# Kernel optimization log

Measured on AMD Instinct MI355X. Metric: run time of the kernel, lower is better.

## Reference

```python
import jax, jax.numpy as jnp
import numpy as np
from jax import lax

N, C_IN, C_OUT, T, V = 16, 256, 256, 300, 25
K = 3            # s_kernel_size
TK = 9           # t_kernel_size
BN_EPS = 1e-5


def setup_inputs() -> dict:
    key = jax.random.key(0)
    ks = jax.random.split(key, 12)
    x = jax.random.normal(ks[0], (N, C_IN, T, V), dtype=jnp.float32)
    A = jax.random.uniform(ks[1], (K, V, V), dtype=jnp.float32)
    att_A = jax.random.uniform(ks[2], (N, 1, V, V), dtype=jnp.float32)  # unused by S_GC
    M = jnp.ones((K, V, V), dtype=jnp.float32)
    # 1x1 spatial conv: out = K*C_OUT channels
    conv_w = jax.random.normal(ks[3], (K * C_OUT, C_IN), dtype=jnp.float32) * 0.02
    conv_b = jnp.zeros((K * C_OUT,), dtype=jnp.float32)
    # BN1 (eval mode)
    bn1_gamma = jnp.ones((C_OUT,), dtype=jnp.float32)
    bn1_beta = jnp.zeros((C_OUT,), dtype=jnp.float32)
    bn1_mean = jax.random.normal(ks[4], (C_OUT,), dtype=jnp.float32) * 0.1
    bn1_var = jax.random.uniform(ks[5], (C_OUT,), dtype=jnp.float32) + 0.5
    # temporal conv: kernel (TK, 1), stride 1, pad ((TK-1)//2, 0)
    tconv_w = jax.random.normal(ks[6], (C_OUT, C_OUT, TK, 1), dtype=jnp.float32) * 0.02
    tconv_b = jnp.zeros((C_OUT,), dtype=jnp.float32)
    # BN2 (eval mode)
    bn2_gamma = jnp.ones((C_OUT,), dtype=jnp.float32)
    bn2_beta = jnp.zeros((C_OUT,), dtype=jnp.float32)
    bn2_mean = jax.random.normal(ks[7], (C_OUT,), dtype=jnp.float32) * 0.1
    bn2_var = jax.random.uniform(ks[8], (C_OUT,), dtype=jnp.float32) + 0.5
    return {
        "x": x, "A": A, "att_A": att_A, "M": M,
        "conv_w": conv_w, "conv_b": conv_b,
        "bn1_gamma": bn1_gamma, "bn1_beta": bn1_beta, "bn1_mean": bn1_mean, "bn1_var": bn1_var,
        "tconv_w": tconv_w, "tconv_b": tconv_b,
        "bn2_gamma": bn2_gamma, "bn2_beta": bn2_beta, "bn2_mean": bn2_mean, "bn2_var": bn2_var,
    }


def _bn(x, gamma, beta, mean, var):
    # eval-mode BatchNorm2d over channel dim of NCHW tensor
    scale = gamma / jnp.sqrt(var + BN_EPS)
    return x * scale[None, :, None, None] + (beta - mean * scale)[None, :, None, None]


def reference(x, A, att_A, M, conv_w, conv_b,
              bn1_gamma, bn1_beta, bn1_mean, bn1_var,
              tconv_w, tconv_b,
              bn2_gamma, bn2_beta, bn2_mean, bn2_var):
    # --- S_GC: 1x1 conv -> view (n,K,c,t,v) -> einsum with A*M ---
    y = jnp.einsum('nctv,oc->notv', x, conv_w) + conv_b[None, :, None, None]
    y = y.reshape(N, K, C_OUT, T, V)
    sgc = jnp.einsum('nkctv,kvw->nctw', y, A * M)
    # --- tgc: BN -> ReLU -> temporal conv -> BN -> Dropout(0) -> ReLU ---
    h = jax.nn.relu(_bn(sgc, bn1_gamma, bn1_beta, bn1_mean, bn1_var))
    h = lax.conv_general_dilated(
        h, tconv_w, window_strides=(1, 1),
        padding=(((TK - 1) // 2, (TK - 1) // 2), (0, 0)),
        dimension_numbers=('NCHW', 'OIHW', 'NCHW'))
    h = h + tconv_b[None, :, None, None]
    h = jax.nn.relu(_bn(h, bn2_gamma, bn2_beta, bn2_mean, bn2_var))
    # --- residual: identity (in_channels == out_channels, stride == 1) ---
    return h + x
```

## Files before the change

kernel.cpp:

```cpp
#include <hip/hip_runtime.h>
#include <math.h>

constexpr int TVL = 7500;
constexpr int CIN = 256;
constexpr int CO  = 256;
constexpr int KO  = 768;
constexpr int KK3 = 2304;
#define BNEPS 1e-5f

typedef __attribute__((ext_vector_type(8))) short short8;
typedef __attribute__((ext_vector_type(4))) float f32x4;
typedef unsigned short ushortT;

static __device__ __forceinline__ ushortT f2bf(float v) {
    unsigned x = __float_as_uint(v);
    unsigned r = (x + 0x7fffu + ((x >> 16) & 1u)) >> 16;
    return (ushortT)r;
}
static __device__ __forceinline__ float bf2f(ushortT u) {
    return __uint_as_float((unsigned)u << 16);
}

static __device__ __forceinline__ void gll16(const void* g, void* l) {
    __builtin_amdgcn_global_load_lds(
        (const __attribute__((address_space(1))) void*)g,
        (__attribute__((address_space(3))) void*)l, 16, 0, 0);
}

__global__ void ksplit_w1(const float* __restrict__ w,
                          ushortT* __restrict__ dH, ushortT* __restrict__ dL,
                          ushortT* __restrict__ zb)
{
    if (blockIdx.x == 0 && threadIdx.x < 16) zb[threadIdx.x] = 0;
    int i = blockIdx.x * 256 + threadIdx.x;
    if (i < KO * CIN) {
        float v = w[i];
        ushortT h = f2bf(v);
        dH[i] = h;
        dL[i] = f2bf(v - bf2f(h));
    }
}

__global__ void ksplit_w3(const float* __restrict__ w,
                          ushortT* __restrict__ dH, ushortT* __restrict__ dL)
{
    int i = blockIdx.x * 256 + threadIdx.x;
    if (i < CO * KK3) {
        int o = i / KK3, rem = i - o * KK3;
        int c = rem / 9, dt = rem - c * 9;
        float v = w[i];
        ushortT h = f2bf(v);
        int j = o * KK3 + dt * 256 + c;
        dH[j] = h;
        dL[j] = f2bf(v - bf2f(h));
    }
}

__global__ __launch_bounds__(256) void ktrans_split(
    const float* __restrict__ src, ushortT* __restrict__ dH, ushortT* __restrict__ dL)
{
    __shared__ float tile[32][33];
    const int z = blockIdx.z;
    src += (size_t)z * CO * TVL;
    dH  += (size_t)z * TVL * 256;
    dL  += (size_t)z * TVL * 256;
    const int tx = threadIdx.x & 31, ty = threadIdx.x >> 5;
    const int wBase = blockIdx.x * 32, cBase = blockIdx.y * 32;
    #pragma unroll
    for (int i = 0; i < 4; ++i) {
        int r = ty + i * 8;
        int w = wBase + tx;
        tile[r][tx] = (w < TVL) ? src[(size_t)(cBase + r) * TVL + w] : 0.f;
    }
    __syncthreads();
    #pragma unroll
    for (int i = 0; i < 4; ++i) {
        int wr = ty + i * 8;
        int w = wBase + wr;
        if (w < TVL) {
            float v = tile[tx][wr];
            ushortT hi = f2bf(v);
            ushortT lo = f2bf(v - bf2f(hi));
            dH[(size_t)w * 256 + cBase + tx] = hi;
            dL[(size_t)w * 256 + cBase + tx] = lo;
        }
    }
}

__global__ __launch_bounds__(256) void k1_mfma(
    const ushortT* __restrict__ Wh, const ushortT* __restrict__ Wl,
    const ushortT* __restrict__ Xh, const ushortT* __restrict__ Xl,
    const ushortT* __restrict__ zb,
    const float* __restrict__ bias, float* __restrict__ out1)
{
    __shared__ __align__(16) short Ah[4096], Al[4096], Bh[4096], Bl[4096];
    const int tid = threadIdx.x;
    const int ng = blockIdx.z;
    const int rowBase = blockIdx.y * 128;
    const int colBase = blockIdx.x * 128;
    const ushortT* XhN = Xh + (size_t)ng * TVL * 256;
    const ushortT* XlN = Xl + (size_t)ng * TVL * 256;

    f32x4 acc[4][4];
    #pragma unroll
    for (int a = 0; a < 4; ++a)
        #pragma unroll
        for (int b = 0; b < 4; ++b) acc[a][b] = (f32x4){0.f, 0.f, 0.f, 0.f};

    const int r0 = tid >> 2, s = tid & 3;
    const int wv = tid >> 6, lane = tid & 63;
    const int wy = wv >> 1, wx = wv & 1;
    const int q = lane >> 4, l15 = lane & 15;
    const int qs0 = s ^ ((r0 >> 1) & 3);
    const int qsr = q ^ ((l15 >> 1) & 3);
    const int ldo0 = tid * 16, ldo1 = 4096 + tid * 16;
    const int bcol0 = colBase + r0, bcol1 = colBase + r0 + 64;

    #pragma unroll 1
    for (int kk = 0; kk < CIN; kk += 32) {
        const size_t goA = (size_t)(rowBase + r0) * CIN + kk + qs0 * 8;
        gll16(Wh + goA, (char*)Ah + ldo0);
        gll16(Wl + goA, (char*)Al + ldo0);
        gll16(Wh + goA + (size_t)64 * CIN, (char*)Ah + ldo1);
        gll16(Wl + goA + (size_t)64 * CIN, (char*)Al + ldo1);

        const size_t goB0 = (size_t)bcol0 * 256 + kk + qs0 * 8;
        const size_t goB1 = (size_t)bcol1 * 256 + kk + qs0 * 8;
        gll16(bcol0 < TVL ? (const void*)(XhN + goB0) : (const void*)zb, (char*)Bh + ldo0);
        gll16(bcol0 < TVL ? (const void*)(XlN + goB0) : (const void*)zb, (char*)Bl + ldo0);
        gll16(bcol1 < TVL ? (const void*)(XhN + goB1) : (const void*)zb, (char*)Bh + ldo1);
        gll16(bcol1 < TVL ? (const void*)(XlN + goB1) : (const void*)zb, (char*)Bl + ldo1);
        __syncthreads();

        short8 ah[4], al[4], bh[4], bl[4];
        #pragma unroll
        for (int mi = 0; mi < 4; ++mi) {
            const int off = (wy * 64 + mi * 16 + l15) * 64 + qsr * 16;
            ah[mi] = *(const short8*)((const char*)Ah + off);
            al[mi] = *(const short8*)((const char*)Al + off);
        }
        #pragma unroll
        for (int ni = 0; ni < 4; ++ni) {
            const int off = (wx * 64 + ni * 16 + l15) * 64 + qsr * 16;
            bh[ni] = *(const short8*)((const char*)Bh + off);
            bl[ni] = *(const short8*)((const char*)Bl + off);
        }
        #pragma unroll
        for (int mi = 0; mi < 4; ++mi)
            #pragma unroll
            for (int ni = 0; ni < 4; ++ni) {
                acc[mi][ni] = __builtin_amdgcn_mfma_f32_16x16x32_bf16(ah[mi], bh[ni], acc[mi][ni], 0, 0, 0);
                acc[mi][ni] = __builtin_amdgcn_mfma_f32_16x16x32_bf16(ah[mi], bl[ni], acc[mi][ni], 0, 0, 0);
                acc[mi][ni] = __builtin_amdgcn_mfma_f32_16x16x32_bf16(al[mi], bh[ni], acc[mi][ni], 0, 0, 0);
            }
        __syncthreads();
    }

    float* out1n = out1 + (size_t)ng * KO * TVL;
    #pragma unroll
    for (int mi = 0; mi < 4; ++mi)
        #pragma unroll
        for (int rr = 0; rr < 4; ++rr) {
            const int row = rowBase + wy * 64 + mi * 16 + q * 4 + rr;
            const float bv = bias[row];
            #pragma unroll
            for (int ni = 0; ni < 4; ++ni) {
                const int col = colBase + wx * 64 + ni * 16 + l15;
                if (col < TVL)
                    out1n[(size_t)row * TVL + col] = acc[mi][ni][rr] + bv;
            }
        }
}

__global__ __launch_bounds__(256) void k2_sgc(
    const float* __restrict__ out1, const float* __restrict__ A,
    const float* __restrict__ Mm, const float* __restrict__ g1,
    const float* __restrict__ b1, const float* __restrict__ m1,
    const float* __restrict__ v1, float* __restrict__ h)
{
    __shared__ __align__(16) float AMs[3 * 25 * 28];
    const int tid = threadIdx.x;
    for (int i = tid; i < 1875; i += 256)
        AMs[(i / 25) * 28 + (i % 25)] = A[i] * Mm[i];
    __syncthreads();

    const int r  = blockIdx.x * 256 + tid;
    const int t2 = r % 150;
    const int rc = r / 150;
    const int c  = rc & 255;
    const int ng = rc >> 8;
    const int t  = t2 * 2;

    const float* base = out1 + ((size_t)ng * KO + c) * TVL + t * 25;
    float o0[25], o1[25];
    #pragma unroll
    for (int w = 0; w < 25; ++w) { o0[w] = 0.f; o1[w] = 0.f; }

    for (int k = 0; k < 3; ++k) {
        const float* yp = base + (size_t)k * CO * TVL;
        float y0[25], y1[25];
        #pragma unroll
        for (int v = 0; v < 25; ++v) { y0[v] = yp[v]; y1[v] = yp[25 + v]; }
        const float* amk = &AMs[k * 25 * 28];
        for (int v = 0; v < 25; ++v) {
            const float* am = amk + v * 28;
            const float ya = y0[v], yb = y1[v];
            #pragma unroll
            for (int w = 0; w < 25; ++w) {
                const float a = am[w];
                o0[w] += ya * a;
                o1[w] += yb * a;
            }
        }
    }

    const float sc = g1[c] / sqrtf(v1[c] + BNEPS);
    const float bi = b1[c] - m1[c] * sc;
    float* hp = h + ((size_t)ng * CO + c) * TVL + t * 25;
    #pragma unroll
    for (int w = 0; w < 25; ++w) {
        const float va = o0[w] * sc + bi;
        const float vb = o1[w] * sc + bi;
        hp[w]      = va > 0.f ? va : 0.f;
        hp[25 + w] = vb > 0.f ? vb : 0.f;
    }
}

__global__ __launch_bounds__(256) void k3_mfma(
    const ushortT* __restrict__ Wh, const ushortT* __restrict__ Wl,
    const ushortT* __restrict__ Hh, const ushortT* __restrict__ Hl,
    const ushortT* __restrict__ zb,
    const float* __restrict__ tb, const float* __restrict__ g2,
    const float* __restrict__ b2, const float* __restrict__ m2,
    const float* __restrict__ v2, const float* __restrict__ x,
    float* __restrict__ out, int n0)
{
    __shared__ __align__(16) short Ah[4096], Al[4096], Bh[4096], Bl[4096];
    const int tid = threadIdx.x;
    const int ng = blockIdx.z;
    const int rowBase = blockIdx.y * 128;
    const int colBase = blockIdx.x * 128;
    const ushortT* HhN = Hh + (size_t)ng * TVL * 256;
    const ushortT* HlN = Hl + (size_t)ng * TVL * 256;

    f32x4 acc[4][4];
    #pragma unroll
    for (int a = 0; a < 4; ++a)
        #pragma unroll
        for (int b = 0; b < 4; ++b) acc[a][b] = (f32x4){0.f, 0.f, 0.f, 0.f};

    const int r0 = tid >> 2, s = tid & 3;
    const int wv = tid >> 6, lane = tid & 63;
    const int wy = wv >> 1, wx = wv & 1;
    const int q = lane >> 4, l15 = lane & 15;
    const int qs0 = s ^ ((r0 >> 1) & 3);
    const int qsr = q ^ ((l15 >> 1) & 3);
    const int ldo0 = tid * 16, ldo1 = 4096 + tid * 16;
    const int bcol0 = colBase + r0, bcol1 = colBase + r0 + 64;

    #pragma unroll 1
    for (int kk = 0; kk < KK3; kk += 32) {
        const int dt = kk >> 8;
        const int c0 = kk & 255;
        const int shift = dt * 25 - 100;

        const size_t goA = (size_t)(rowBase + r0) * KK3 + kk + qs0 * 8;
        gll16(Wh + goA, (char*)Ah + ldo0);
        gll16(Wl + goA, (char*)Al + ldo0);
        gll16(Wh + goA + (size_t)64 * KK3, (char*)Ah + ldo1);
        gll16(Wl + goA + (size_t)64 * KK3, (char*)Al + ldo1);

        const int gcol0 = bcol0 + shift, gcol1 = bcol1 + shift;
        const bool ok0 = (bcol0 < TVL) && ((unsigned)gcol0 < (unsigned)TVL);
        const bool ok1 = (bcol1 < TVL) && ((unsigned)gcol1 < (unsigned)TVL);
        const size_t goB0 = (size_t)gcol0 * 256 + c0 + qs0 * 8;
        const size_t goB1 = (size_t)gcol1 * 256 + c0 + qs0 * 8;
        gll16(ok0 ? (const void*)(HhN + goB0) : (const void*)zb, (char*)Bh + ldo0);
        gll16(ok0 ? (const void*)(HlN + goB0) : (const void*)zb, (char*)Bl + ldo0);
        gll16(ok1 ? (const void*)(HhN + goB1) : (const void*)zb, (char*)Bh + ldo1);
        gll16(ok1 ? (const void*)(HlN + goB1) : (const void*)zb, (char*)Bl + ldo1);
        __syncthreads();

        short8 ah[4], al[4], bh[4], bl[4];
        #pragma unroll
        for (int mi = 0; mi < 4; ++mi) {
            const int off = (wy * 64 + mi * 16 + l15) * 64 + qsr * 16;
            ah[mi] = *(const short8*)((const char*)Ah + off);
            al[mi] = *(const short8*)((const char*)Al + off);
        }
        #pragma unroll
        for (int ni = 0; ni < 4; ++ni) {
            const int off = (wx * 64 + ni * 16 + l15) * 64 + qsr * 16;
            bh[ni] = *(const short8*)((const char*)Bh + off);
            bl[ni] = *(const short8*)((const char*)Bl + off);
        }
        #pragma unroll
        for (int mi = 0; mi < 4; ++mi)
            #pragma unroll
            for (int ni = 0; ni < 4; ++ni) {
                acc[mi][ni] = __builtin_amdgcn_mfma_f32_16x16x32_bf16(ah[mi], bh[ni], acc[mi][ni], 0, 0, 0);
                acc[mi][ni] = __builtin_amdgcn_mfma_f32_16x16x32_bf16(ah[mi], bl[ni], acc[mi][ni], 0, 0, 0);
                acc[mi][ni] = __builtin_amdgcn_mfma_f32_16x16x32_bf16(al[mi], bh[ni], acc[mi][ni], 0, 0, 0);
            }
        __syncthreads();
    }

    const float* xn = x   + (size_t)(n0 + ng) * CO * TVL;
    float*       on = out + (size_t)(n0 + ng) * CO * TVL;
    #pragma unroll
    for (int mi = 0; mi < 4; ++mi)
        #pragma unroll
        for (int rr = 0; rr < 4; ++rr) {
            const int row = rowBase + wy * 64 + mi * 16 + q * 4 + rr;
            const float sc = g2[row] / sqrtf(v2[row] + BNEPS);
            const float bb = (tb[row] - m2[row]) * sc + b2[row];
            #pragma unroll
            for (int ni = 0; ni < 4; ++ni) {
                const int col = colBase + wx * 64 + ni * 16 + l15;
                if (col < TVL) {
                    const size_t o = (size_t)row * TVL + col;
                    on[o] = fmaxf(acc[mi][ni][rr] * sc + bb, 0.f) + xn[o];
                }
            }
        }
}

extern "C" void kernel_launch(void* const* d_in, const int* in_sizes, int n_in,
                              void* d_out, int out_size, void* d_ws, size_t ws_size,
                              hipStream_t stream)
{
    const float* x  = (const float*)d_in[0];
    const float* A  = (const float*)d_in[1];
    const float* Mm = (const float*)d_in[3];
    const float* cw = (const float*)d_in[4];
    const float* cb = (const float*)d_in[5];
    const float* g1 = (const float*)d_in[6];
    const float* b1 = (const float*)d_in[7];
    const float* m1 = (const float*)d_in[8];
    const float* v1 = (const float*)d_in[9];
    const float* tw = (const float*)d_in[10];
    const float* tb = (const float*)d_in[11];
    const float* g2 = (const float*)d_in[12];
    const float* b2 = (const float*)d_in[13];
    const float* m2 = (const float*)d_in[14];
    const float* v2 = (const float*)d_in[15];
    float* out = (float*)d_out;

    ushortT* zb  = (ushortT*)d_ws;
    ushortT* W1h = (ushortT*)((char*)d_ws + 256);
    ushortT* W1l = W1h + KO * CIN;
    ushortT* W3h = W1l + KO * CIN;
    ushortT* W3l = W3h + CO * KK3;
    char* dyn = (char*)(W3l + CO * KK3);
    const size_t fixed = (size_t)(dyn - (char*)d_ws);
    const size_t avail = ws_size > fixed ? ws_size - fixed : 0;
    const size_t perN = (size_t)KO * TVL * 4 + (size_t)CO * TVL * 4
                      + 4 * (size_t)TVL * 256 * 2;
    int g = 16;
    while (g > 1 && (size_t)g * perN > avail) g >>= 1;

    float*   out1 = (float*)dyn;
    float*   hbuf = out1 + (size_t)g * KO * TVL;
    ushortT* Hh   = (ushortT*)(hbuf + (size_t)g * CO * TVL);
    ushortT* Hl   = Hh + (size_t)g * TVL * 256;
    ushortT* Xh   = Hl + (size_t)g * TVL * 256;
    ushortT* Xl   = Xh + (size_t)g * TVL * 256;

    hipLaunchKernelGGL(ksplit_w1, dim3((KO * CIN + 255) / 256), dim3(256), 0, stream, cw, W1h, W1l, zb);
    hipLaunchKernelGGL(ksplit_w3, dim3((CO * KK3 + 255) / 256), dim3(256), 0, stream, tw, W3h, W3l);

    for (int n0 = 0; n0 < 16; n0 += g) {
        hipLaunchKernelGGL(ktrans_split, dim3(235, 8, g), dim3(256), 0, stream,
                           x + (size_t)n0 * CIN * TVL, Xh, Xl);
        hipLaunchKernelGGL(k1_mfma, dim3(59, 6, g), dim3(256), 0, stream,
                           W1h, W1l, Xh, Xl, zb, cb, out1);
        hipLaunchKernelGGL(k2_sgc, dim3(g * 150), dim3(256), 0, stream,
                           out1, A, Mm, g1, b1, m1, v1, hbuf);
        hipLaunchKernelGGL(ktrans_split, dim3(235, 8, g), dim3(256), 0, stream,
                           hbuf, Hh, Hl);
        hipLaunchKernelGGL(k3_mfma, dim3(59, 2, g), dim3(256), 0, stream,
                           W3h, W3l, Hh, Hl, zb, tb, g2, b2, m2, v2, x, out, n0);
    }
}
```

Before: 1.318 ms.

## Double-buffer LDS in MFMA GEMMs, remap blocks across XCDs, reuse workspace buffers

Both bf16x3 MFMA GEMM kernels now use double-buffered LDS: the next K-slice is loaded with global_load_lds while the current slice is computed, which hides load latency and needs one fewer barrier per step. Block indices are remapped so consecutive tiles land on the same XCD, which should improve L2 reuse. k2 writes its output in place into out1 and the transposed H reuses the X split buffers, shrinking the per-batch workspace so larger groups fit. The in-place write drops the restrict qualifiers and relies on each thread reading its inputs before writing, and doubling LDS to 64KB per block may lower occupancy.

```diff
diff --git a/kernel.cpp b/kernel.cpp
--- a/kernel.cpp
+++ b/kernel.cpp
@@ -25,6 +25,21 @@
     __builtin_amdgcn_global_load_lds(
         (const __attribute__((address_space(1))) void*)g,
         (__attribute__((address_space(3))) void*)l, 16, 0, 0);
+}
+
+static __device__ __forceinline__ void xcd_remap(int gx, int gy,
+                                                 int& bx, int& by, int& bz)
+{
+    const int gz = gridDim.z;
+    const int total = gx * gy * gz;
+    const int lin = blockIdx.x + gx * (blockIdx.y + gy * blockIdx.z);
+    const int q = total >> 3, r = total & 7;
+    const int xcd = lin & 7, idx = lin >> 3;
+    const int nl = (xcd < r ? xcd * (q + 1) : r * (q + 1) + (xcd - r) * q) + idx;
+    bx = nl % gx;
+    const int rest = nl / gx;
+    by = rest % gy;
+    bz = rest / gy;
 }
 
 __global__ void ksplit_w1(const float* __restrict__ w,
@@ -57,11 +72,12 @@
 }
 
 __global__ __launch_bounds__(256) void ktrans_split(
-    const float* __restrict__ src, ushortT* __restrict__ dH, ushortT* __restrict__ dL)
+    const float* __restrict__ src, size_t zstr,
+    ushortT* __restrict__ dH, ushortT* __restrict__ dL)
 {
     __shared__ float tile[32][33];
     const int z = blockIdx.z;
-    src += (size_t)z * CO * TVL;
+    src += (size_t)z * zstr;
     dH  += (size_t)z * TVL * 256;
     dL  += (size_t)z * TVL * 256;
     const int tx = threadIdx.x & 31, ty = threadIdx.x >> 5;
@@ -93,11 +109,13 @@
     const ushortT* __restrict__ zb,
     const float* __restrict__ bias, float* __restrict__ out1)
 {
-    __shared__ __align__(16) short Ah[4096], Al[4096], Bh[4096], Bl[4096];
+    __shared__ __align__(16) short Ah[2][4096], Al[2][4096], Bh[2][4096], Bl[2][4096];
     const int tid = threadIdx.x;
-    const int ng = blockIdx.z;
-    const int rowBase = blockIdx.y * 128;
-    const int colBase = blockIdx.x * 128;
+    int bx, by, bz;
+    xcd_remap(gridDim.x, gridDim.y, bx, by, bz);
+    const int ng = bz;
+    const int rowBase = by * 128;
+    const int colBase = bx * 128;
     const ushortT* XhN = Xh + (size_t)ng * TVL * 256;
     const ushortT* XlN = Xl + (size_t)ng * TVL * 256;
 
@@ -116,34 +134,46 @@
     const int ldo0 = tid * 16, ldo1 = 4096 + tid * 16;
     const int bcol0 = colBase + r0, bcol1 = colBase + r0 + 64;
 
+    auto stage = [&](int kk, int p) {
+        short* ahp = Ah[p]; short* alp = Al[p];
+        short* bhp = Bh[p]; short* blp = Bl[p];
+        const size_t goA = (size_t)(rowBase + r0) * CIN + kk + qs0 * 8;
+        gll16(Wh + goA, (char*)ahp + ldo0);
+        gll16(Wl + goA, (char*)alp + ldo0);
+        gll16(Wh + goA + (size_t)64 * CIN, (char*)ahp + ldo1);
+        gll16(Wl + goA + (size_t)64 * CIN, (char*)alp + ldo1);
+        const size_t goB0 = (size_t)bcol0 * 256 + kk + qs0 * 8;
+        const size_t goB1 = (size_t)bcol1 * 256 + kk + qs0 * 8;
+        gll16(bcol0 < TVL ? (const void*)(XhN + goB0) : (const void*)zb, (char*)bhp + ldo0);
+        gll16(bcol0 < TVL ? (const void*)(XlN + goB0) : (const void*)zb, (char*)blp + ldo0);
+        gll16(bcol1 < TVL ? (const void*)(XhN + goB1) : (const void*)zb, (char*)bhp + ldo1);
+        gll16(bcol1 < TVL ? (const void*)(XlN + goB1) : (const void*)zb, (char*)blp + ldo1);
+    };
+
+    stage(0, 0);
+    __syncthreads();
+    int p = 0;
+
     #pragma unroll 1
     for (int kk = 0; kk < CIN; kk += 32) {
-        const size_t goA = (size_t)(rowBase + r0) * CIN + kk + qs0 * 8;
-        gll16(Wh + goA, (char*)Ah + ldo0);
-        gll16(Wl + goA, (char*)Al + ldo0);
-        gll16(Wh + goA + (size_t)64 * CIN, (char*)Ah + ldo1);
-        gll16(Wl + goA + (size_t)64 * CIN, (char*)Al + ldo1);
-
-        const size_t goB0 = (size_t)bcol0 * 256 + kk + qs0 * 8;
-        const size_t goB1 = (size_t)bcol1 * 256 + kk + qs0 * 8;
-        gll16(bcol0 < TVL ? (const void*)(XhN + goB0) : (const void*)zb, (char*)Bh + ldo0);
-        gll16(bcol0 < TVL ? (const void*)(XlN + goB0) : (const void*)zb, (char*)Bl + ldo0);
-        gll16(bcol1 < TVL ? (const void*)(XhN + goB1) : (const void*)zb, (char*)Bh + ldo1);
-        gll16(bcol1 < TVL ? (const void*)(XlN + goB1) : (const void*)zb, (char*)Bl + ldo1);
-        __syncthreads();
-
+        if (kk + 32 < CIN) stage(kk + 32, p ^ 1);
+
+        const char* AhP = (const char*)Ah[p];
+        const char* AlP = (const char*)Al[p];
+        const char* BhP = (const char*)Bh[p];
+        const char* BlP = (const char*)Bl[p];
         short8 ah[4], al[4], bh[4], bl[4];
         #pragma unroll
         for (int mi = 0; mi < 4; ++mi) {
             const int off = (wy * 64 + mi * 16 + l15) * 64 + qsr * 16;
-            ah[mi] = *(const short8*)((const char*)Ah + off);
-            al[mi] = *(const short8*)((const char*)Al + off);
+            ah[mi] = *(const short8*)(AhP + off);
+            al[mi] = *(const short8*)(AlP + off);
         }
         #pragma unroll
         for (int ni = 0; ni < 4; ++ni) {
             const int off = (wx * 64 + ni * 16 + l15) * 64 + qsr * 16;
-            bh[ni] = *(const short8*)((const char*)Bh + off);
-            bl[ni] = *(const short8*)((const char*)Bl + off);
+            bh[ni] = *(const short8*)(BhP + off);
+            bl[ni] = *(const short8*)(BlP + off);
         }
         #pragma unroll
         for (int mi = 0; mi < 4; ++mi)
@@ -154,6 +184,7 @@
                 acc[mi][ni] = __builtin_amdgcn_mfma_f32_16x16x32_bf16(al[mi], bh[ni], acc[mi][ni], 0, 0, 0);
             }
         __syncthreads();
+        p ^= 1;
     }
 
     float* out1n = out1 + (size_t)ng * KO * TVL;
@@ -173,10 +204,10 @@
 }
 
 __global__ __launch_bounds__(256) void k2_sgc(
-    const float* __restrict__ out1, const float* __restrict__ A,
+    const float* out1, const float* __restrict__ A,
     const float* __restrict__ Mm, const float* __restrict__ g1,
     const float* __restrict__ b1, const float* __restrict__ m1,
-    const float* __restrict__ v1, float* __restrict__ h)
+    const float* __restrict__ v1, float* h)
 {
     __shared__ __align__(16) float AMs[3 * 25 * 28];
     const int tid = threadIdx.x;
@@ -216,7 +247,7 @@
 
     const float sc = g1[c] / sqrtf(v1[c] + BNEPS);
     const float bi = b1[c] - m1[c] * sc;
-    float* hp = h + ((size_t)ng * CO + c) * TVL + t * 25;
+    float* hp = h + ((size_t)ng * KO + c) * TVL + t * 25;
     #pragma unroll
     for (int w = 0; w < 25; ++w) {
         const float va = o0[w] * sc + bi;
@@ -235,11 +266,13 @@
     const float* __restrict__ v2, const float* __restrict__ x,
     float* __restrict__ out, int n0)
 {
-    __shared__ __align__(16) short Ah[4096], Al[4096], Bh[4096], Bl[4096];
+    __shared__ __align__(16) short Ah[2][4096], Al[2][4096], Bh[2][4096], Bl[2][4096];
     const int tid = threadIdx.x;
-    const int ng = blockIdx.z;
-    const int rowBase = blockIdx.y * 128;
-    const int colBase = blockIdx.x * 128;
+    int bx, by, bz;
+    xcd_remap(gridDim.x, gridDim.y, bx, by, bz);
+    const int ng = bz;
+    const int rowBase = by * 128;
+    const int colBase = bx * 128;
     const ushortT* HhN = Hh + (size_t)ng * TVL * 256;
     const ushortT* HlN = Hl + (size_t)ng * TVL * 256;
 
@@ -258,41 +291,52 @@
     const int ldo0 = tid * 16, ldo1 = 4096 + tid * 16;
     const int bcol0 = colBase + r0, bcol1 = colBase + r0 + 64;
 
-    #pragma unroll 1
-    for (int kk = 0; kk < KK3; kk += 32) {
+    auto stage = [&](int kk, int p) {
+        short* ahp = Ah[p]; short* alp = Al[p];
+        short* bhp = Bh[p]; short* blp = Bl[p];
         const int dt = kk >> 8;
         const int c0 = kk & 255;
         const int shift = dt * 25 - 100;
-
         const size_t goA = (size_t)(rowBase + r0) * KK3 + kk + qs0 * 8;
-        gll16(Wh + goA, (char*)Ah + ldo0);
-        gll16(Wl + goA, (char*)Al + ldo0);
-        gll16(Wh + goA + (size_t)64 * KK3, (char*)Ah + ldo1);
-        gll16(Wl + goA + (size_t)64 * KK3, (char*)Al + ldo1);
-
+        gll16(Wh + goA, (char*)ahp + ldo0);
+        gll16(Wl + goA, (char*)alp + ldo0);
+        gll16(Wh + goA + (size_t)64 * KK3, (char*)ahp + ldo1);
+        gll16(Wl + goA + (size_t)64 * KK3, (char*)alp + ldo1);
         const int gcol0 = bcol0 + shift, gcol1 = bcol1 + shift;
         const bool ok0 = (bcol0 < TVL) && ((unsigned)gcol0 < (unsigned)TVL);
         const bool ok1 = (bcol1 < TVL) && ((unsigned)gcol1 < (unsigned)TVL);
         const size_t goB0 = (size_t)gcol0 * 256 + c0 + qs0 * 8;
         const size_t goB1 = (size_t)gcol1 * 256 + c0 + qs0 * 8;
-        gll16(ok0 ? (const void*)(HhN + goB0) : (const void*)zb, (char*)Bh + ldo0);
-        gll16(ok0 ? (const void*)(HlN + goB0) : (const void*)zb, (char*)Bl + ldo0);
-        gll16(ok1 ? (const void*)(HhN + goB1) : (const void*)zb, (char*)Bh + ldo1);
-        gll16(ok1 ? (const void*)(HlN + goB1) : (const void*)zb, (char*)Bl + ldo1);
-        __syncthreads();
-
+        gll16(ok0 ? (const void*)(HhN + goB0) : (const void*)zb, (char*)bhp + ldo0);
+        gll16(ok0 ? (const void*)(HlN + goB0) : (const void*)zb, (char*)blp + ldo0);
+        gll16(ok1 ? (const void*)(HhN + goB1) : (const void*)zb, (char*)bhp + ldo1);
+        gll16(ok1 ? (const void*)(HlN + goB1) : (const void*)zb, (char*)blp + ldo1);
+    };
+
+    stage(0, 0);
+    __syncthreads();
+    int p = 0;
+
+    #pragma unroll 1
+    for (int kk = 0; kk < KK3; kk += 32) {
+        if (kk + 32 < KK3) stage(kk + 32, p ^ 1);
+
+        const char* AhP = (const char*)Ah[p];
+        const char* AlP = (const char*)Al[p];
+        const char* BhP = (const char*)Bh[p];
+        const char* BlP = (const char*)Bl[p];
         short8 ah[4], al[4], bh[4], bl[4];
         #pragma unroll
         for (int mi = 0; mi < 4; ++mi) {
             const int off = (wy * 64 + mi * 16 + l15) * 64 + qsr * 16;
-            ah[mi] = *(const short8*)((const char*)Ah + off);
-            al[mi] = *(const short8*)((const char*)Al + off);
+            ah[mi] = *(const short8*)(AhP + off);
+            al[mi] = *(const short8*)(AlP + off);
         }
         #pragma unroll
         for (int ni = 0; ni < 4; ++ni) {
             const int off = (wx * 64 + ni * 16 + l15) * 64 + qsr * 16;
-            bh[ni] = *(const short8*)((const char*)Bh + off);
-            bl[ni] = *(const short8*)((const char*)Bl + off);
+            bh[ni] = *(const short8*)(BhP + off);
+            bl[ni] = *(const short8*)(BlP + off);
         }
         #pragma unroll
         for (int mi = 0; mi < 4; ++mi)
@@ -303,6 +347,7 @@
                 acc[mi][ni] = __builtin_amdgcn_mfma_f32_16x16x32_bf16(al[mi], bh[ni], acc[mi][ni], 0, 0, 0);
             }
         __syncthreads();
+        p ^= 1;
     }
 
     const float* xn = x   + (size_t)(n0 + ng) * CO * TVL;
@@ -354,16 +399,12 @@
     char* dyn = (char*)(W3l + CO * KK3);
     const size_t fixed = (size_t)(dyn - (char*)d_ws);
     const size_t avail = ws_size > fixed ? ws_size - fixed : 0;
-    const size_t perN = (size_t)KO * TVL * 4 + (size_t)CO * TVL * 4
-                      + 4 * (size_t)TVL * 256 * 2;
+    const size_t perN = (size_t)KO * TVL * 4 + 2 * (size_t)TVL * 256 * 2;
     int g = 16;
     while (g > 1 && (size_t)g * perN > avail) g >>= 1;
 
     float*   out1 = (float*)dyn;
-    float*   hbuf = out1 + (size_t)g * KO * TVL;
-    ushortT* Hh   = (ushortT*)(hbuf + (size_t)g * CO * TVL);
-    ushortT* Hl   = Hh + (size_t)g * TVL * 256;
-    ushortT* Xh   = Hl + (size_t)g * TVL * 256;
+    ushortT* Xh   = (ushortT*)(out1 + (size_t)g * KO * TVL);
     ushortT* Xl   = Xh + (size_t)g * TVL * 256;
 
     hipLaunchKernelGGL(ksplit_w1, dim3((KO * CIN + 255) / 256), dim3(256), 0, stream, cw, W1h, W1l, zb);
@@ -371,14 +412,14 @@
 
     for (int n0 = 0; n0 < 16; n0 += g) {
         hipLaunchKernelGGL(ktrans_split, dim3(235, 8, g), dim3(256), 0, stream,
-                           x + (size_t)n0 * CIN * TVL, Xh, Xl);
+                           x + (size_t)n0 * CIN * TVL, (size_t)CIN * TVL, Xh, Xl);
         hipLaunchKernelGGL(k1_mfma, dim3(59, 6, g), dim3(256), 0, stream,
                            W1h, W1l, Xh, Xl, zb, cb, out1);
         hipLaunchKernelGGL(k2_sgc, dim3(g * 150), dim3(256), 0, stream,
-                           out1, A, Mm, g1, b1, m1, v1, hbuf);
+                           out1, A, Mm, g1, b1, m1, v1, out1 );
         hipLaunchKernelGGL(ktrans_split, dim3(235, 8, g), dim3(256), 0, stream,
-                           hbuf, Hh, Hl);
+                           out1, (size_t)KO * TVL, Xh, Xl);
         hipLaunchKernelGGL(k3_mfma, dim3(59, 2, g), dim3(256), 0, stream,
-                           W3h, W3l, Hh, Hl, zb, tb, g2, b2, m2, v2, x, out, n0);
-    }
-}
+                           W3h, W3l, Xh, Xl, zb, tb, g2, b2, m2, v2, x, out, n0);
+    }
+}
```

Result: faster. 1.250 ms (-5.1%).
